# Kernel tuning notes

Measured on AMD Instinct MI355X. Metric: run time of the kernel, lower is better.

## Reference

```python
import jax, jax.numpy as jnp
import numpy as np

B, N, NB, NORB = 8, 128, 32, 128  # batch, particles, single-body basis size, orbitals


def _offdiag_idx(n):
    # [N, N-1] indices of j != i, matching remove_diag with an aux (feature) axis
    return np.stack([np.concatenate([np.arange(i), np.arange(i + 1, n)]) for i in range(n)])


def setup_inputs() -> dict:
    key = jax.random.key(0)
    k1, k2 = jax.random.split(key)
    chi = jax.random.normal(k1, (B, N, NB), dtype=jnp.float32)
    # param('backflow_coeff', normal(stddev=0.01), (Nb*Nb, n_orbitals))
    backflow_coeff = 0.01 * jax.random.normal(k2, (NB * NB, NORB), dtype=jnp.float32)
    return {"chi": chi, "backflow_coeff": backflow_coeff}


def reference(chi, backflow_coeff):
    b, n, nb = chi.shape
    # basis_combine_backflow: chi_munu_ij[b,i,j, k*Nb + l] = chi[b,j,k] * chi[b,i,l]
    # (meshgrid(a=chi_i, b=chi_j) with indexing='xy' -> prod[k,l] = chi_i[l]*chi_j[k], raveled)
    pair = jnp.einsum('bjk,bil->bijkl', chi, chi).reshape(b, n, n, nb * nb)
    # remove_diag(..., has_aux_axis=True): drop j == i along axis 2 -> [B, N, N-1, Nb^2]
    idx = jnp.asarray(_offdiag_idx(n))
    pair = pair[:, jnp.arange(n)[:, None], idx, :]
    # mean over neighbors j != i -> [B, N, Nb^2]
    basis = pair.mean(axis=-2)
    # BF = basis @ backflow_coeff -> [B, N, n_orbitals]
    return basis @ backflow_coeff
```

## Files before the change

### kernel.cpp

```cpp
#include <hip/hip_runtime.h>

#define B_    8
#define N_    128
#define NB_   32
#define NORB_ 128
#define RPB   8
#define OPB   16
#define THREADS 256
#define RPAD  18

__global__ __launch_bounds__(THREADS, 4) void bobf_kernel(
    const float* __restrict__ chi,
    const float* __restrict__ W,
    float* __restrict__ out)
{
    __shared__ float Sp[8][NB_];
    __shared__ float S[NB_];
    __shared__ __align__(16) float xT[NB_][RPB];
    __shared__ __align__(16) float red[32][RPB][RPAD];

    const int t   = threadIdx.x;
    const int blk = blockIdx.x;
    const int b    = blk >> 7;
    const int rowg = (blk >> 3) & 15;
    const int og   = blk & 7;
    const int i0   = rowg * RPB;
    const int o0   = og * OPB;

    {
        const int k = t & 31;
        const int g = t >> 5;
        const float* base = chi + (b * N_) * NB_ + k;
        float s = 0.f;
        #pragma unroll
        for (int jj = 0; jj < 16; ++jj) s += base[(g * 16 + jj) * NB_];
        Sp[g][k] = s;
    }
    {
        const int r = t >> 5, l = t & 31;
        xT[l][r] = chi[(b * N_ + i0 + r) * NB_ + l];
    }
    __syncthreads();
    if (t < NB_) {
        float s = 0.f;
        #pragma unroll
        for (int g = 0; g < 8; ++g) s += Sp[g][t];
        S[t] = s;
    }
    __syncthreads();

    const int q  = t >> 3;
    const int rg = (t >> 2) & 1;
    const int oq = t & 3;
    const int r0 = rg * 4;

    const float inv = 1.0f / (float)(N_ - 1);
    float4 yv;
    {
        const float4 xq = *(const float4*)&xT[q][r0];
        const float Sq = S[q];
        yv.x = (Sq - xq.x) * inv;
        yv.y = (Sq - xq.y) * inv;
        yv.z = (Sq - xq.z) * inv;
        yv.w = (Sq - xq.w) * inv;
    }

    const float4* Wf  = (const float4*)(W + (q * 32) * NORB_ + o0 + oq * 4);
    const float*  xjp = &xT[0][r0];

    float4 a0 = {0,0,0,0}, a1 = {0,0,0,0}, a2 = {0,0,0,0}, a3 = {0,0,0,0};
    #pragma unroll 8
    for (int j = 0; j < 32; ++j) {
        const float4 xv = *(const float4*)(xjp + j * RPB);
        const float4 wv = Wf[j * (NORB_ / 4)];
        const float p0 = yv.x * xv.x;
        const float p1 = yv.y * xv.y;
        const float p2 = yv.z * xv.z;
        const float p3 = yv.w * xv.w;
        a0.x += p0 * wv.x; a0.y += p0 * wv.y; a0.z += p0 * wv.z; a0.w += p0 * wv.w;
        a1.x += p1 * wv.x; a1.y += p1 * wv.y; a1.z += p1 * wv.z; a1.w += p1 * wv.w;
        a2.x += p2 * wv.x; a2.y += p2 * wv.y; a2.z += p2 * wv.z; a2.w += p2 * wv.w;
        a3.x += p3 * wv.x; a3.y += p3 * wv.y; a3.z += p3 * wv.z; a3.w += p3 * wv.w;
    }

    {
        float* rq = &red[q][0][0] + oq * 4;
        *(float4*)&rq[(r0 + 0) * RPAD] = a0;
        *(float4*)&rq[(r0 + 1) * RPAD] = a1;
        *(float4*)&rq[(r0 + 2) * RPAD] = a2;
        *(float4*)&rq[(r0 + 3) * RPAD] = a3;
    }
    __syncthreads();
    if (t < RPB * OPB) {
        const int r = t >> 4, o = t & 15;
        float v = 0.f;
        #pragma unroll
        for (int qq = 0; qq < 32; ++qq) v += red[qq][r][o];
        out[(b * N_ + i0 + r) * NORB_ + o0 + o] = v;
    }
}

extern "C" void kernel_launch(void* const* d_in, const int* in_sizes, int n_in,
                              void* d_out, int out_size, void* d_ws, size_t ws_size,
                              hipStream_t stream) {
    const float* chi = (const float*)d_in[0];
    const float* W   = (const float*)d_in[1];
    float* out = (float*)d_out;
    dim3 grid(1024);
    dim3 block(THREADS);
    hipLaunchKernelGGL(bobf_kernel, grid, block, 0, stream, chi, W, out);
}
```

Before: 11.99 us.

## Double threads per block, drop shared xT staging, load chi rows into registers

Raises the block size to 512 threads, so each thread handles 2 rows instead of 4 and the column-sum phase uses 16 partial groups. The shared transpose buffer xT and one barrier are removed. Each thread now loads its two chi rows straight from global memory into register arrays, and the y term is computed from global reads. The aim is more parallelism and fewer LDS round trips and syncs, at the cost of more register pressure and redundant global loads.

```diff
diff --git a/kernel.cpp b/kernel.cpp
--- a/kernel.cpp
+++ b/kernel.cpp
@@ -6,7 +6,7 @@
 #define NORB_ 128
 #define RPB   8
 #define OPB   16
-#define THREADS 256
+#define THREADS 512
 #define RPAD  18
 
 __global__ __launch_bounds__(THREADS, 4) void bobf_kernel(
@@ -14,9 +14,8 @@
     const float* __restrict__ W,
     float* __restrict__ out)
 {
-    __shared__ float Sp[8][NB_];
+    __shared__ float Sp[16][NB_];
     __shared__ float S[NB_];
-    __shared__ __align__(16) float xT[NB_][RPB];
     __shared__ __align__(16) float red[32][RPB][RPAD];
 
     const int t   = threadIdx.x;
@@ -33,62 +32,52 @@
         const float* base = chi + (b * N_) * NB_ + k;
         float s = 0.f;
         #pragma unroll
-        for (int jj = 0; jj < 16; ++jj) s += base[(g * 16 + jj) * NB_];
+        for (int jj = 0; jj < 8; ++jj) s += base[(g * 8 + jj) * NB_];
         Sp[g][k] = s;
-    }
-    {
-        const int r = t >> 5, l = t & 31;
-        xT[l][r] = chi[(b * N_ + i0 + r) * NB_ + l];
     }
     __syncthreads();
     if (t < NB_) {
         float s = 0.f;
         #pragma unroll
-        for (int g = 0; g < 8; ++g) s += Sp[g][t];
+        for (int g = 0; g < 16; ++g) s += Sp[g][t];
         S[t] = s;
     }
-    __syncthreads();
 
-    const int q  = t >> 3;
-    const int rg = (t >> 2) & 1;
+    const int q  = t >> 4;
+    const int r0 = ((t >> 2) & 3) * 2;
     const int oq = t & 3;
-    const int r0 = rg * 4;
 
-    const float inv = 1.0f / (float)(N_ - 1);
-    float4 yv;
-    {
-        const float4 xq = *(const float4*)&xT[q][r0];
-        const float Sq = S[q];
-        yv.x = (Sq - xq.x) * inv;
-        yv.y = (Sq - xq.y) * inv;
-        yv.z = (Sq - xq.z) * inv;
-        yv.w = (Sq - xq.w) * inv;
+    const float* row0 = chi + (b * N_ + i0 + r0) * NB_;
+    const float* row1 = row0 + NB_;
+    float x0s[32], x1s[32];
+    #pragma unroll
+    for (int u = 0; u < 8; ++u) {
+        const float4 v0 = ((const float4*)row0)[u];
+        const float4 v1 = ((const float4*)row1)[u];
+        x0s[u * 4 + 0] = v0.x; x0s[u * 4 + 1] = v0.y; x0s[u * 4 + 2] = v0.z; x0s[u * 4 + 3] = v0.w;
+        x1s[u * 4 + 0] = v1.x; x1s[u * 4 + 1] = v1.y; x1s[u * 4 + 2] = v1.z; x1s[u * 4 + 3] = v1.w;
     }
 
-    const float4* Wf  = (const float4*)(W + (q * 32) * NORB_ + o0 + oq * 4);
-    const float*  xjp = &xT[0][r0];
+    __syncthreads();
+    const float inv = 1.0f / (float)(N_ - 1);
+    const float y0 = (S[q] - row0[q]) * inv;
+    const float y1 = (S[q] - row1[q]) * inv;
 
-    float4 a0 = {0,0,0,0}, a1 = {0,0,0,0}, a2 = {0,0,0,0}, a3 = {0,0,0,0};
-    #pragma unroll 8
+    const float* Wp = W + (q * 32) * NORB_ + o0 + oq * 4;
+    float4 a0 = {0,0,0,0}, a1 = {0,0,0,0};
+    #pragma unroll
     for (int j = 0; j < 32; ++j) {
-        const float4 xv = *(const float4*)(xjp + j * RPB);
-        const float4 wv = Wf[j * (NORB_ / 4)];
-        const float p0 = yv.x * xv.x;
-        const float p1 = yv.y * xv.y;
-        const float p2 = yv.z * xv.z;
-        const float p3 = yv.w * xv.w;
+        const float4 wv = *(const float4*)(Wp + j * NORB_);
+        const float p0 = y0 * x0s[j];
+        const float p1 = y1 * x1s[j];
         a0.x += p0 * wv.x; a0.y += p0 * wv.y; a0.z += p0 * wv.z; a0.w += p0 * wv.w;
         a1.x += p1 * wv.x; a1.y += p1 * wv.y; a1.z += p1 * wv.z; a1.w += p1 * wv.w;
-        a2.x += p2 * wv.x; a2.y += p2 * wv.y; a2.z += p2 * wv.z; a2.w += p2 * wv.w;
-        a3.x += p3 * wv.x; a3.y += p3 * wv.y; a3.z += p3 * wv.z; a3.w += p3 * wv.w;
     }
 
     {
-        float* rq = &red[q][0][0] + oq * 4;
-        *(float4*)&rq[(r0 + 0) * RPAD] = a0;
-        *(float4*)&rq[(r0 + 1) * RPAD] = a1;
-        *(float4*)&rq[(r0 + 2) * RPAD] = a2;
-        *(float4*)&rq[(r0 + 3) * RPAD] = a3;
+        float* rq = &red[q][r0][oq * 4];
+        *(float4*)rq = a0;
+        *(float4*)(rq + RPAD) = a1;
     }
     __syncthreads();
     if (t < RPB * OPB) {
```

Result: slower. 18.63 us (+55.4%).
